# Kernel optimization log

Hardware: AMD Instinct MI355X
Metric: run time of the kernel (lower is better)

Reference implementation:

```python
import jax, jax.numpy as jnp
import numpy as np

# Module hyperparameters (from init_kwargs)
P = 96                 # num_of_patches
W = 1536.0             # input width
H = 1536.0             # input height
XPS = W / P            # x patch size = 16
YPS = H / P            # y patch size = 16
PROB_THR = 0.9
IOU_THR = 0.5
N = P * P              # total candidate boxes


def setup_inputs() -> dict:
    key = jax.random.key(0)
    # x: [5, P, P] -> channel 0 = probability, 1..4 = (x, y, w, h) in [0,1)
    x = jax.random.uniform(key, (5, P, P), dtype=jnp.float32)
    return {"x": x}


def _pairwise_iou(b):
    # b: [N, 4] xyxy
    x1, y1, x2, y2 = b[:, 0], b[:, 1], b[:, 2], b[:, 3]
    area = (x2 - x1) * (y2 - y1)                       # [N]
    ix1 = jnp.maximum(x1[:, None], x1[None, :])
    iy1 = jnp.maximum(y1[:, None], y1[None, :])
    ix2 = jnp.minimum(x2[:, None], x2[None, :])
    iy2 = jnp.minimum(y2[:, None], y2[None, :])
    inter = jnp.clip(ix2 - ix1, 0.0) * jnp.clip(iy2 - iy1, 0.0)
    union = area[:, None] + area[None, :] - inter
    return jnp.where(union > 0, inter / union, 0.0)    # [N, N]


def _forward(x):
    # --- scale_batch_bbx_xywh, applied densely (invalid entries are masked later) ---
    p = x[0]
    ii = jnp.arange(P, dtype=x.dtype)[:, None]   # row index i
    jj = jnp.arange(P, dtype=x.dtype)[None, :]   # col index j
    bx = x[1] * XPS + ii * XPS
    by = x[2] * YPS + jj * YPS
    bw = x[3] * W
    bh = x[4] * H
    bbx = jnp.stack([p, bx, by, bw, bh], axis=0).reshape(5, N).T   # [N, 5] (p, x, y, w, h)

    # --- remove_low_probability_bbx: fixed-shape validity mask instead of filtering ---
    scores = bbx[:, 0]
    valid = scores > PROB_THR

    # --- convert_batch_to_xyxy + round ---
    x1 = jnp.round(bbx[:, 1])
    y1 = jnp.round(bbx[:, 2])
    x2 = jnp.round(bbx[:, 3] + bbx[:, 1])
    y2 = jnp.round(bbx[:, 4] + bbx[:, 2])

    # --- greedy NMS (torchvision semantics): sort by score desc, suppress by IoU ---
    sort_key = jnp.where(valid, scores, -jnp.inf)
    order = jnp.argsort(-sort_key)
    boxes = jnp.stack([x1, y1, x2, y2], axis=1)[order]   # [N, 4] sorted
    sc = scores[order]
    v = valid[order]
    iou = _pairwise_iou(boxes)                           # [N, N]

    def body(kept, i):
        suppressed = jnp.any(kept & (iou[i] > IOU_THR))
        ki = v[i] & ~suppressed
        return kept.at[i].set(ki), ki

    _, keeps = jax.lax.scan(body, jnp.zeros((N,), bool), jnp.arange(N))

    # --- cat([scores, bbx]) then convert_batch_to_xywh on kept rows ---
    out = jnp.stack(
        [sc, boxes[:, 0], boxes[:, 1], boxes[:, 2] - boxes[:, 0], boxes[:, 3] - boxes[:, 1]],
        axis=1,
    )  # [N, 5] = (score, x, y, w, h), score-descending order like nms output
    out = jnp.where(keeps[:, None], out, 0.0)
    return out, keeps


def reference(x):
    # Returns (out [N,5], keep_mask [N]); rows with keep_mask=False are zeroed.
    # This is the fixed-shape equivalent of the variable-length torch output.
    return _forward(x)
```

## Files before the change

### kernel.cpp

```cpp
#include <hip/hip_runtime.h>

#define PP 96
#define NB (PP*PP)
#define NCH (NB/64)
#define PROB_THR 0.9f
#define FAST_CAP 1024
#define LSTRIDE 1034

typedef unsigned long long u64;
typedef unsigned int u32;

__device__ __forceinline__ void decode_core(int n, float xv, float yv, float wv, float hv,
                                            float& X1, float& Y1, float& X2, float& Y2)
{
    int i = n / PP;
    int j = n - i * PP;
    float bx = __fadd_rn(__fmul_rn(xv, 16.0f), (float)i * 16.0f);
    float by = __fadd_rn(__fmul_rn(yv, 16.0f), (float)j * 16.0f);
    float bw = __fmul_rn(wv, 1536.0f);
    float bh = __fmul_rn(hv, 1536.0f);
    X1 = rintf(bx);
    Y1 = rintf(by);
    X2 = rintf(__fadd_rn(bw, bx));
    Y2 = rintf(__fadd_rn(bh, by));
}

__device__ __forceinline__ void decode_box(const float* __restrict__ x, int n,
                                           float& X1, float& Y1, float& X2, float& Y2)
{
    decode_core(n, x[NB + n], x[2 * NB + n], x[3 * NB + n], x[4 * NB + n], X1, Y1, X2, Y2);
}

__device__ __forceinline__ int iou_hit_nodiv(float ix1, float iy1, float ix2, float iy2, float iar,
                                             float jx1, float jy1, float jx2, float jy2, float jar)
{
    float xx1 = fmaxf(ix1, jx1), yy1 = fmaxf(iy1, jy1);
    float xx2 = fminf(ix2, jx2), yy2 = fminf(iy2, jy2);
    float iw = fmaxf(__fsub_rn(xx2, xx1), 0.0f);
    float ih = fmaxf(__fsub_rn(yy2, yy1), 0.0f);
    float inter = __fmul_rn(iw, ih);
    float uni = __fsub_rn(__fadd_rn(iar, jar), inter);
    return (uni > 0.0f && __fadd_rn(inter, inter) > uni) ? 1 : 0;
}

__device__ __forceinline__ int iou_hit_div(float ix1, float iy1, float ix2, float iy2, float iar,
                                           float jx1, float jy1, float jx2, float jy2, float jar)
{
    float xx1 = fmaxf(ix1, jx1), yy1 = fmaxf(iy1, jy1);
    float xx2 = fminf(ix2, jx2), yy2 = fminf(iy2, jy2);
    float iw = fmaxf(__fsub_rn(xx2, xx1), 0.0f);
    float ih = fmaxf(__fsub_rn(yy2, yy1), 0.0f);
    float inter = __fmul_rn(iw, ih);
    float uni = __fsub_rn(__fadd_rn(iar, jar), inter);
    return (uni > 0.0f && __fdiv_rn(inter, uni) > 0.5f) ? 1 : 0;
}

__global__ void __launch_bounds__(512) k_sort(
    const float* __restrict__ x,
    float* __restrict__ gss, float4* __restrict__ gbox,
    u64* __restrict__ skeys, int* __restrict__ counter, int ws_ok)
{
    __shared__ u64 lmask[NCH];
    __shared__ int pc[NCH], loff[NCH];
    __shared__ int sM;
    __shared__ u64 kdb[FAST_CAP];

    const int tid = threadIdx.x;
    const int lane = tid & 63;
    const int wv = tid >> 6;

    #pragma unroll
    for (int g = 0; g < 18; g += 6) {
        float sv[6];
        #pragma unroll
        for (int u = 0; u < 6; ++u)
            sv[u] = x[((wv + ((g + u) << 3)) << 6) + lane];
        #pragma unroll
        for (int u = 0; u < 6; ++u) {
            u64 m = __ballot(sv[u] > PROB_THR);
            if (lane == 0) lmask[wv + ((g + u) << 3)] = m;
        }
    }
    __syncthreads();
    if (tid < NCH) pc[tid] = __popcll(lmask[tid]);
    __syncthreads();
    if (tid < 64) {
        int acc = 0;
        for (int seg = 0; seg < 3; ++seg) {
            int c = (seg << 6) + lane;
            int pv = (c < NCH) ? pc[c] : 0;
            int v = pv;
            #pragma unroll
            for (int off = 1; off < 64; off <<= 1) {
                int u = __shfl_up(v, off);
                if (lane >= off) v += u;
            }
            if (c < NCH) loff[c] = acc + v - pv;
            acc += __shfl(v, 63);
        }
        if (lane == 0) sM = acc;
    }
    __syncthreads();
    const int M = sM;
    const bool fast = (M <= FAST_CAP) && ws_ok;
    if (tid == 0) counter[0] = M;

    if (!fast) {
        for (int c = wv; c < NCH; c += 8) {
            float s = x[(c << 6) + lane];
            u64 m = lmask[c];
            if ((m >> lane) & 1ull) {
                int pos = loff[c] + __popcll(m & ((1ull << lane) - 1ull));
                int n = (c << 6) + lane;
                skeys[pos] = ((u64)__float_as_uint(s) << 32) | (u64)(NB - 1 - n);
            }
        }
        return;
    }

    for (int c = wv; c < NCH; c += 8) {
        float s = x[(c << 6) + lane];
        u64 m = lmask[c];
        if ((m >> lane) & 1ull) {
            int pos = loff[c] + __popcll(m & ((1ull << lane) - 1ull));
            int n = (c << 6) + lane;
            kdb[pos] = ((u64)__float_as_uint(s) << 32) | (u64)(NB - 1 - n);
        }
    }
    for (int q = M + tid; q < FAST_CAP; q += 512) kdb[q] = 0ull;
    __syncthreads();

    u64 k0 = kdb[tid], k1 = kdb[tid + 512];
    int n0 = NB - 1 - (int)(k0 & 0xFFFFFFFFull);
    int n1 = NB - 1 - (int)(k1 & 0xFFFFFFFFull);
    float xv0 = x[NB + n0], yv0 = x[2 * NB + n0], wv0 = x[3 * NB + n0], hv0 = x[4 * NB + n0];
    float xv1 = x[NB + n1], yv1 = x[2 * NB + n1], wv1 = x[3 * NB + n1], hv1 = x[4 * NB + n1];
    int r0 = 0, r1 = 0;
    const int nck = (M + 63) >> 6;
    for (int ch = 0; ch < nck; ++ch) {
        u64 kq = kdb[(ch << 6) + lane];
        u32 qlo = (u32)kq, qhi = (u32)(kq >> 32);
        #pragma unroll
        for (int i = 0; i < 64; ++i) {
            u32 blo = (u32)__builtin_amdgcn_readlane((int)qlo, i);
            u32 bhi = (u32)__builtin_amdgcn_readlane((int)qhi, i);
            u64 kb = ((u64)bhi << 32) | (u64)blo;
            r0 += (kb > k0) ? 1 : 0;
            r1 += (kb > k1) ? 1 : 0;
        }
    }
    if (tid < M) {
        float X1, Y1, X2, Y2;
        decode_core(n0, xv0, yv0, wv0, hv0, X1, Y1, X2, Y2);
        gbox[r0] = make_float4(X1, Y1, X2, Y2);
        gss[r0] = __uint_as_float((u32)(k0 >> 32));
    }
    if (tid + 512 < M) {
        float X1, Y1, X2, Y2;
        decode_core(n1, xv1, yv1, wv1, hv1, X1, Y1, X2, Y2);
        gbox[r1] = make_float4(X1, Y1, X2, Y2);
        gss[r1] = __uint_as_float((u32)(k1 >> 32));
    }
}

__global__ void __launch_bounds__(256) k_adj(
    float* __restrict__ out, const float4* __restrict__ gbox,
    const int* __restrict__ counter, u64* __restrict__ adjT, int ws_ok)
{
    __shared__ float4 lb[FAST_CAP];
    __shared__ float la[FAST_CAP];
    int M = counter[0]; if (M > NB) M = NB;
    const int tid = threadIdx.x, lane = tid & 63, wv = tid >> 6, b = blockIdx.x;

    float4 z4 = make_float4(0.f, 0.f, 0.f, 0.f);
    for (int q = tid; q < 216; q += 256)
        ((float4*)out)[b * 216 + q] = z4;

    const bool fast = (M <= FAST_CAP) && ws_ok;
    if (!fast) return;
    if ((b << 4) >= M) return;

    const int W = (M + 63) >> 6;
    for (int f = tid; f < M; f += 256) {
        float4 bb = gbox[f];
        lb[f] = bb;
        la[f] = __fmul_rn(__fsub_rn(bb.z, bb.x), __fsub_rn(bb.w, bb.y));
    }
    __syncthreads();

    #pragma unroll
    for (int r = 0; r < 4; ++r) {
        int i = (b << 4) + (r << 2) + wv;
        if (i >= M) break;
        float4 bi = lb[i];
        float iar = la[i];
        for (int kk = 0; kk < W; ++kk) {
            int j = (kk << 6) + lane;
            float4 bj = lb[j & (FAST_CAP - 1)];
            float jar = la[j & (FAST_CAP - 1)];
            int hit = (j < M) && iou_hit_nodiv(bi.x, bi.y, bi.z, bi.w, iar,
                                               bj.x, bj.y, bj.z, bj.w, jar);
            u64 mm = __ballot(hit);
            if (lane == 0) adjT[((size_t)kk << 10) + i] = mm;
        }
    }
}

#define SUBCHUNK(DSRC)                                                        \
    {                                                                         \
        const ulonglong2* cp2 = (const ulonglong2*)(Lds + cbase + (sc << 3)); \
        const ulonglong2* rp2 = (const ulonglong2*)(Lds + rbase + (sc << 3)); \
        ulonglong2 ca = cp2[0], cb = cp2[1], cc = cp2[2], cd = cp2[3];        \
        ulonglong2 ra = rp2[0], rbv = rp2[1], rc = rp2[2], rd = rp2[3];       \
        u64 colb[8] = {ca.x, ca.y, cb.x, cb.y, cc.x, cc.y, cd.x, cd.y};       \
        u64 rowb[8] = {ra.x, ra.y, rbv.x, rbv.y, rc.x, rc.y, rd.x, rd.y};     \
        _Pragma("unroll")                                                     \
        for (int t = 0; t < 8; ++t) {                                         \
            const int bitp = (sc << 3) + t;                                   \
            u32 bbit = ((DSRC) >> bitp) & 1u;                                 \
            u32 m = bbit - 1u;                     \
            dl |= (u32)colb[t] & m;                                           \
            dh |= (u32)(colb[t] >> 32) & m;                                   \
            supl |= (u32)rowb[t] & m;                                         \
            suph |= (u32)(rowb[t] >> 32) & m;                                 \
            kw |= m & (1u << bitp);                                           \
        }                                                                     \
    }

__global__ void __launch_bounds__(256) k_sweep(
    const float* __restrict__ x, float* __restrict__ out,
    float* __restrict__ gss, float4* __restrict__ gbox,
    const u64* __restrict__ skeys, const int* __restrict__ counter,
    const u64* __restrict__ adjT, int ws_ok)
{
    __shared__ __align__(16) u64 Lds[16 * LSTRIDE];
    __shared__ u64 keepw[NCH];
    int M = counter[0]; if (M > NB) M = NB;
    const int W = (M + 63) >> 6;
    const bool fast = (M <= FAST_CAP) && ws_ok;
    const int tid = threadIdx.x, lane = tid & 63;

    if (fast) {
        const int npair = W << 9;
        const ulonglong2* gp = (const ulonglong2*)adjT;
        for (int r = 0; r < 4; ++r) {
            int fb = (r << 11) + tid;
            ulonglong2 v[8];
            #pragma unroll
            for (int u = 0; u < 8; ++u) {
                int f = fb + (u << 8);
                v[u] = (f < npair) ? gp[f] : make_ulonglong2(0ull, 0ull);
            }
            #pragma unroll
            for (int u = 0; u < 8; ++u) {
                int f = fb + (u << 8);
                if (f < npair) {
                    int w = f >> 9, r2 = f & 511;
                    ((ulonglong2*)Lds)[w * (LSTRIDE >> 1) + r2] = v[u];
                }
            }
        }
        __syncthreads();

        if (tid < 64) {
            const int wl = (lane < W) ? lane : 0;
            u32 supl = 0u, suph = 0u, dl = 0u, dh = 0u;
            u64 mykw = 0ull;
            const int nrb = (M + 31) >> 5;
            for (int rb = 0; rb < nrb; ++rb) {
                const int c = rb >> 1;
                const int base = rb << 5;
                const size_t cbase = (size_t)c * LSTRIDE + base;
                const size_t rbase = (size_t)wl * LSTRIDE + base;
                if (!(rb & 1)) {
                    if (rb == 0) { dl = 0u; dh = 0u; }
                    else { dl = (u32)__shfl((int)supl, c); dh = (u32)__shfl((int)suph, c); }
                    int rem = M - (c << 6);
                    if (rem < 64) {
                        if (rem >= 32) dh |= 0xFFFFFFFFu << (rem - 32);
                        else { dh = 0xFFFFFFFFu; dl |= 0xFFFFFFFFu << rem; }
                    }
                }
                u32 kw = 0u;
                if (!(rb & 1)) {
                    #pragma unroll
                    for (int sc = 0; sc < 4; ++sc) SUBCHUNK(dl)
                } else {
                    #pragma unroll
                    for (int sc = 0; sc < 4; ++sc) SUBCHUNK(dh)
                }
                mykw |= (lane == c) ? ((u64)kw << ((rb & 1) << 5)) : 0ull;
            }
            keepw[lane] = mykw;
        }
    } else {
        for (int t = tid; t < M; t += 256) {
            u64 key = skeys[t];
            int r = 0;
            for (int q = 0; q < M; ++q) r += (skeys[q] > key) ? 1 : 0;
            int n = NB - 1 - (int)(key & 0xFFFFFFFFull);
            float X1, Y1, X2, Y2;
            decode_box(x, n, X1, Y1, X2, Y2);
            gbox[r] = make_float4(X1, Y1, X2, Y2);
            gss[r] = __uint_as_float((u32)(key >> 32));
        }
        __threadfence();
        __syncthreads();
        if (tid < 64) {
            u64 kbs[3] = {0ull, 0ull, 0ull};
            for (int i = 0; i < M; ++i) {
                float4 bi = gbox[i];
                float iar = __fmul_rn(__fsub_rn(bi.z, bi.x), __fsub_rn(bi.w, bi.y));
                int hit = 0;
                int nk = (i > lane) ? ((i - lane + 63) >> 6) : 0;
                for (int w = 0; w < 3 && !hit; ++w) {
                    int klim = nk - (w << 6);
                    if (klim <= 0) break;
                    u64 bits = kbs[w];
                    if (klim < 64) bits &= ((1ull << klim) - 1ull);
                    while (bits) {
                        int kk2 = __builtin_ctzll(bits);
                        bits &= bits - 1ull;
                        int jj = lane + (((w << 6) + kk2) << 6);
                        float4 bj = gbox[jj];
                        float jar = __fmul_rn(__fsub_rn(bj.z, bj.x), __fsub_rn(bj.w, bj.y));
                        if (iou_hit_div(bi.x, bi.y, bi.z, bi.w, iar,
                                        bj.x, bj.y, bj.z, bj.w, jar)) { hit = 1; break; }
                    }
                }
                int suppressed = __any(hit);
                if (!suppressed && lane == (i & 63)) kbs[(i >> 6) >> 6] |= 1ull << ((i >> 6) & 63);
            }
            int NWrd = (M + 63) >> 6;
            for (int wd = 0; wd < NWrd; ++wd) {
                u64 bit = (kbs[wd >> 6] >> (wd & 63)) & 1ull;
                u64 word = __ballot(bit != 0);
                if (lane == 0 && wd < NCH) keepw[wd] = word;
            }
        }
    }
    __syncthreads();

    for (int i = tid; i < M; i += 256) {
        if ((keepw[i >> 6] >> (i & 63)) & 1ull) {
            float4 bb = gbox[i];
            out[i * 5 + 0] = gss[i];
            out[i * 5 + 1] = bb.x;
            out[i * 5 + 2] = bb.y;
            out[i * 5 + 3] = __fsub_rn(bb.z, bb.x);
            out[i * 5 + 4] = __fsub_rn(bb.w, bb.y);
            out[5 * NB + i] = 1.0f;
        }
    }
}

extern "C" void kernel_launch(void* const* d_in, const int* in_sizes, int n_in,
                              void* d_out, int out_size, void* d_ws, size_t ws_size,
                              hipStream_t stream) {
    const float* x = (const float*)d_in[0];
    float* out = (float*)d_out;

    char* ws = (char*)d_ws;
    int* counter = (int*)ws;
    float*  gss  = (float*)(ws + 16);
    float4* gbox = (float4*)(ws + 16 + (size_t)4 * NB);
    u64*    adjT = (u64*)(ws + 16 + (size_t)4 * NB + (size_t)16 * NB);
    u64*    skeys = (u64*)((char*)adjT + (size_t)16384 * 8);
    const size_t NEEDED = 16 + (size_t)4 * NB + (size_t)16 * NB
                        + (size_t)16384 * 8 + (size_t)8 * NB;
    int ws_ok = (ws_size >= NEEDED) ? 1 : 0;

    k_sort<<<1, 512, 0, stream>>>(x, gss, gbox, skeys, counter, ws_ok);
    k_adj<<<64, 256, 0, stream>>>(out, gbox, counter, adjT, ws_ok);
    k_sweep<<<1, 256, 0, stream>>>(x, out, gss, gbox, skeys, counter, adjT, ws_ok);
}
```

Baseline: 119.0 us.

## Split rank sort across blocks, widen sweep block, restructure suppression row merge

```diff
diff --git a/kernel.cpp b/kernel.cpp
--- a/kernel.cpp
+++ b/kernel.cpp
@@ -55,7 +55,7 @@
     return (uni > 0.0f && __fdiv_rn(inter, uni) > 0.5f) ? 1 : 0;
 }
 
-__global__ void __launch_bounds__(512) k_sort(
+__global__ void __launch_bounds__(256) k_sort(
     const float* __restrict__ x,
     float* __restrict__ gss, float4* __restrict__ gbox,
     u64* __restrict__ skeys, int* __restrict__ counter, int ws_ok)
@@ -64,21 +64,23 @@
     __shared__ int pc[NCH], loff[NCH];
     __shared__ int sM;
     __shared__ u64 kdb[FAST_CAP];
+    __shared__ int prank[256];
 
     const int tid = threadIdx.x;
     const int lane = tid & 63;
     const int wv = tid >> 6;
+    const int b = blockIdx.x;
 
     #pragma unroll
-    for (int g = 0; g < 18; g += 6) {
+    for (int g = 0; g < 36; g += 6) {
         float sv[6];
         #pragma unroll
         for (int u = 0; u < 6; ++u)
-            sv[u] = x[((wv + ((g + u) << 3)) << 6) + lane];
+            sv[u] = x[((wv * 36 + g + u) << 6) + lane];
         #pragma unroll
         for (int u = 0; u < 6; ++u) {
             u64 m = __ballot(sv[u] > PROB_THR);
-            if (lane == 0) lmask[wv + ((g + u) << 3)] = m;
+            if (lane == 0) lmask[wv * 36 + g + u] = m;
         }
     }
     __syncthreads();
@@ -103,22 +105,24 @@
     __syncthreads();
     const int M = sM;
     const bool fast = (M <= FAST_CAP) && ws_ok;
-    if (tid == 0) counter[0] = M;
+    if (b == 0 && tid == 0) counter[0] = M;
 
     if (!fast) {
-        for (int c = wv; c < NCH; c += 8) {
-            float s = x[(c << 6) + lane];
-            u64 m = lmask[c];
-            if ((m >> lane) & 1ull) {
-                int pos = loff[c] + __popcll(m & ((1ull << lane) - 1ull));
-                int n = (c << 6) + lane;
-                skeys[pos] = ((u64)__float_as_uint(s) << 32) | (u64)(NB - 1 - n);
+        if (b == 0) {
+            for (int c = wv; c < NCH; c += 4) {
+                float s = x[(c << 6) + lane];
+                u64 m = lmask[c];
+                if ((m >> lane) & 1ull) {
+                    int pos = loff[c] + __popcll(m & ((1ull << lane) - 1ull));
+                    int n = (c << 6) + lane;
+                    skeys[pos] = ((u64)__float_as_uint(s) << 32) | (u64)(NB - 1 - n);
+                }
             }
         }
         return;
     }
 
-    for (int c = wv; c < NCH; c += 8) {
+    for (int c = wv; c < NCH; c += 4) {
         float s = x[(c << 6) + lane];
         u64 m = lmask[c];
         if ((m >> lane) & 1ull) {
@@ -127,17 +131,17 @@
             kdb[pos] = ((u64)__float_as_uint(s) << 32) | (u64)(NB - 1 - n);
         }
     }
-    for (int q = M + tid; q < FAST_CAP; q += 512) kdb[q] = 0ull;
-    __syncthreads();
-
-    u64 k0 = kdb[tid], k1 = kdb[tid + 512];
-    int n0 = NB - 1 - (int)(k0 & 0xFFFFFFFFull);
-    int n1 = NB - 1 - (int)(k1 & 0xFFFFFFFFull);
-    float xv0 = x[NB + n0], yv0 = x[2 * NB + n0], wv0 = x[3 * NB + n0], hv0 = x[4 * NB + n0];
-    float xv1 = x[NB + n1], yv1 = x[2 * NB + n1], wv1 = x[3 * NB + n1], hv1 = x[4 * NB + n1];
-    int r0 = 0, r1 = 0;
+    for (int q = M + tid; q < FAST_CAP; q += 256) kdb[q] = 0ull;
+    __syncthreads();
+
+    const int cand = (b << 6) + lane;
+    const u64 k0 = kdb[cand];
+    const int n0 = NB - 1 - (int)(k0 & 0xFFFFFFFFull);
+    float xv0 = x[NB + n0], yv0 = x[2 * NB + n0];
+    float wv0 = x[3 * NB + n0], hv0 = x[4 * NB + n0];
+    int r = 0;
     const int nck = (M + 63) >> 6;
-    for (int ch = 0; ch < nck; ++ch) {
+    for (int ch = wv; ch < nck; ch += 4) {
         u64 kq = kdb[(ch << 6) + lane];
         u32 qlo = (u32)kq, qhi = (u32)(kq >> 32);
         #pragma unroll
@@ -145,21 +149,17 @@
             u32 blo = (u32)__builtin_amdgcn_readlane((int)qlo, i);
             u32 bhi = (u32)__builtin_amdgcn_readlane((int)qhi, i);
             u64 kb = ((u64)bhi << 32) | (u64)blo;
-            r0 += (kb > k0) ? 1 : 0;
-            r1 += (kb > k1) ? 1 : 0;
-        }
-    }
-    if (tid < M) {
+            r += (kb > k0) ? 1 : 0;
+        }
+    }
+    prank[tid] = r;
+    __syncthreads();
+    if (tid < 64 && cand < M) {
+        int rk = prank[tid] + prank[64 + tid] + prank[128 + tid] + prank[192 + tid];
         float X1, Y1, X2, Y2;
         decode_core(n0, xv0, yv0, wv0, hv0, X1, Y1, X2, Y2);
-        gbox[r0] = make_float4(X1, Y1, X2, Y2);
-        gss[r0] = __uint_as_float((u32)(k0 >> 32));
-    }
-    if (tid + 512 < M) {
-        float X1, Y1, X2, Y2;
-        decode_core(n1, xv1, yv1, wv1, hv1, X1, Y1, X2, Y2);
-        gbox[r1] = make_float4(X1, Y1, X2, Y2);
-        gss[r1] = __uint_as_float((u32)(k1 >> 32));
+        gbox[rk] = make_float4(X1, Y1, X2, Y2);
+        gss[rk] = __uint_as_float((u32)(k0 >> 32));
     }
 }
 
@@ -206,28 +206,7 @@
     }
 }
 
-#define SUBCHUNK(DSRC)                                                        \
-    {                                                                         \
-        const ulonglong2* cp2 = (const ulonglong2*)(Lds + cbase + (sc << 3)); \
-        const ulonglong2* rp2 = (const ulonglong2*)(Lds + rbase + (sc << 3)); \
-        ulonglong2 ca = cp2[0], cb = cp2[1], cc = cp2[2], cd = cp2[3];        \
-        ulonglong2 ra = rp2[0], rbv = rp2[1], rc = rp2[2], rd = rp2[3];       \
-        u64 colb[8] = {ca.x, ca.y, cb.x, cb.y, cc.x, cc.y, cd.x, cd.y};       \
-        u64 rowb[8] = {ra.x, ra.y, rbv.x, rbv.y, rc.x, rc.y, rd.x, rd.y};     \
-        _Pragma("unroll")                                                     \
-        for (int t = 0; t < 8; ++t) {                                         \
-            const int bitp = (sc << 3) + t;                                   \
-            u32 bbit = ((DSRC) >> bitp) & 1u;                                 \
-            u32 m = bbit - 1u;                     \
-            dl |= (u32)colb[t] & m;                                           \
-            dh |= (u32)(colb[t] >> 32) & m;                                   \
-            supl |= (u32)rowb[t] & m;                                         \
-            suph |= (u32)(rowb[t] >> 32) & m;                                 \
-            kw |= m & (1u << bitp);                                           \
-        }                                                                     \
-    }
-
-__global__ void __launch_bounds__(256) k_sweep(
+__global__ void __launch_bounds__(1024) k_sweep(
     const float* __restrict__ x, float* __restrict__ out,
     float* __restrict__ gss, float4* __restrict__ gbox,
     const u64* __restrict__ skeys, const int* __restrict__ counter,
@@ -243,21 +222,18 @@
     if (fast) {
         const int npair = W << 9;
         const ulonglong2* gp = (const ulonglong2*)adjT;
-        for (int r = 0; r < 4; ++r) {
-            int fb = (r << 11) + tid;
-            ulonglong2 v[8];
-            #pragma unroll
-            for (int u = 0; u < 8; ++u) {
-                int f = fb + (u << 8);
-                v[u] = (f < npair) ? gp[f] : make_ulonglong2(0ull, 0ull);
-            }
-            #pragma unroll
-            for (int u = 0; u < 8; ++u) {
-                int f = fb + (u << 8);
-                if (f < npair) {
-                    int w = f >> 9, r2 = f & 511;
-                    ((ulonglong2*)Lds)[w * (LSTRIDE >> 1) + r2] = v[u];
-                }
+        ulonglong2 v[8];
+        #pragma unroll
+        for (int u = 0; u < 8; ++u) {
+            int f = tid + (u << 10);
+            v[u] = (f < npair) ? gp[f] : make_ulonglong2(0ull, 0ull);
+        }
+        #pragma unroll
+        for (int u = 0; u < 8; ++u) {
+            int f = tid + (u << 10);
+            if (f < npair) {
+                int w = f >> 9, r2 = f & 511;
+                ((ulonglong2*)Lds)[w * (LSTRIDE >> 1) + r2] = v[u];
             }
         }
         __syncthreads();
@@ -270,8 +246,8 @@
             for (int rb = 0; rb < nrb; ++rb) {
                 const int c = rb >> 1;
                 const int base = rb << 5;
-                const size_t cbase = (size_t)c * LSTRIDE + base;
-                const size_t rbase = (size_t)wl * LSTRIDE + base;
+                const u64* crow = Lds + (size_t)c * LSTRIDE + base;
+                const u64* rrow = Lds + (size_t)wl * LSTRIDE + base;
                 if (!(rb & 1)) {
                     if (rb == 0) { dl = 0u; dh = 0u; }
                     else { dl = (u32)__shfl((int)supl, c); dh = (u32)__shfl((int)suph, c); }
@@ -281,20 +257,46 @@
                         else { dh = 0xFFFFFFFFu; dl |= 0xFFFFFFFFu << rem; }
                     }
                 }
+                u64 colb[32];
+                #pragma unroll
+                for (int q = 0; q < 16; ++q) {
+                    ulonglong2 t2 = ((const ulonglong2*)crow)[q];
+                    colb[2 * q] = t2.x; colb[2 * q + 1] = t2.y;
+                }
                 u32 kw = 0u;
                 if (!(rb & 1)) {
                     #pragma unroll
-                    for (int sc = 0; sc < 4; ++sc) SUBCHUNK(dl)
+                    for (int t = 0; t < 32; ++t) {
+                        u32 bbit = (dl >> t) & 1u;
+                        u32 m = bbit - 1u;
+                        dl |= (u32)colb[t] & m;
+                        dh |= (u32)(colb[t] >> 32) & m;
+                        kw |= m & (1u << t);
+                    }
                 } else {
                     #pragma unroll
-                    for (int sc = 0; sc < 4; ++sc) SUBCHUNK(dh)
+                    for (int t = 0; t < 32; ++t) {
+                        u32 bbit = (dh >> t) & 1u;
+                        u32 m = bbit - 1u;
+                        dl |= (u32)colb[t] & m;
+                        dh |= (u32)(colb[t] >> 32) & m;
+                        kw |= m & (1u << t);
+                    }
+                }
+                u32 bits = kw;
+                while (bits) {
+                    int t = __builtin_ctz(bits);
+                    bits &= bits - 1u;
+                    u64 rv = rrow[t];
+                    supl |= (u32)rv;
+                    suph |= (u32)(rv >> 32);
                 }
                 mykw |= (lane == c) ? ((u64)kw << ((rb & 1) << 5)) : 0ull;
             }
             keepw[lane] = mykw;
         }
     } else {
-        for (int t = tid; t < M; t += 256) {
+        for (int t = tid; t < M; t += 1024) {
             u64 key = skeys[t];
             int r = 0;
             for (int q = 0; q < M; ++q) r += (skeys[q] > key) ? 1 : 0;
@@ -341,7 +343,7 @@
     }
     __syncthreads();
 
-    for (int i = tid; i < M; i += 256) {
+    for (int i = tid; i < M; i += 1024) {
         if ((keepw[i >> 6] >> (i & 63)) & 1ull) {
             float4 bb = gbox[i];
             out[i * 5 + 0] = gss[i];
@@ -370,7 +372,7 @@
                         + (size_t)16384 * 8 + (size_t)8 * NB;
     int ws_ok = (ws_size >= NEEDED) ? 1 : 0;
 
-    k_sort<<<1, 512, 0, stream>>>(x, gss, gbox, skeys, counter, ws_ok);
+    k_sort<<<16, 256, 0, stream>>>(x, gss, gbox, skeys, counter, ws_ok);
     k_adj<<<64, 256, 0, stream>>>(out, gbox, counter, adjT, ws_ok);
-    k_sweep<<<1, 256, 0, stream>>>(x, out, gss, gbox, skeys, counter, adjT, ws_ok);
-}
+    k_sweep<<<1, 1024, 0, stream>>>(x, out, gss, gbox, skeys, counter, adjT, ws_ok);
+}
```

After: 112.3 us. -5.6%, faster.
